# Optimization experiments

Hardware: AMD Instinct MI355X
Metric: run time of the kernel (lower is better)

Reference implementation:

```python
import jax, jax.numpy as jnp
import numpy as np

N = 100000     # nodes
H = 128        # hidden_channels == in_channels
OUT = 64       # out_channels
L = 3          # num_layers=4 -> num_layers-1 Layer modules
E = 1_600_000  # unique undirected edges (avg degree 16)
BN_EPS = 1e-5


def _make_edges():
    # Unique undirected edges, no self-loops -> dense symmetric adjacency in the
    # original module is exactly this edge set symmetrized.
    rng = np.random.default_rng(0)
    i = rng.integers(0, N, 1_700_000)
    j = rng.integers(0, N, 1_700_000)
    m = i != j
    i, j = i[m], j[m]
    lo, hi = np.minimum(i, j), np.maximum(i, j)
    pairs = np.unique(lo.astype(np.int64) * N + hi)[:E]
    lo = (pairs // N).astype(np.int32)
    hi = (pairs % N).astype(np.int32)
    src = jnp.asarray(np.concatenate([lo, hi]))  # [2E] directed
    dst = jnp.asarray(np.concatenate([hi, lo]))
    return src, dst


def setup_inputs() -> dict:
    key = jax.random.key(0)
    ks = jax.random.split(key, 24)
    nrm = lambda k, s: (jax.random.normal(k, s, dtype=jnp.float32) * 0.05)
    src, dst = _make_edges()
    return {
        "x": jax.random.normal(ks[0], (N, H), dtype=jnp.float32),
        "src": src,
        "dst": dst,
        # per-Layer MLP(in=H, hidden=H, out=H): Linear->ReLU->Linear, stacked over L
        "layer_W1": nrm(ks[1], (L, H, H)),
        "layer_b1": nrm(ks[2], (L, H)),
        "layer_W2": nrm(ks[3], (L, H, H)),
        "layer_b2": nrm(ks[4], (L, H)),
        # BatchNorm1d (eval mode: running stats)
        "bn_gamma": 1.0 + nrm(ks[5], (L, H)),
        "bn_beta": nrm(ks[6], (L, H)),
        "bn_mean": nrm(ks[7], (L, H)),
        "bn_var": jax.random.uniform(ks[8], (L, H), jnp.float32, 0.5, 1.5),
        # single shared GRUCell(H, H)
        "gru_Wih": nrm(ks[9], (3 * H, H)),
        "gru_Whh": nrm(ks[10], (3 * H, H)),
        "gru_bih": nrm(ks[11], (3 * H,)),
        "gru_bhh": nrm(ks[12], (3 * H,)),
        # mlp_last: MLP(H, H, OUT)
        "last_W1": nrm(ks[13], (H, H)),
        "last_b1": nrm(ks[14], (H,)),
        "last_W2": nrm(ks[15], (OUT, H)),
        "last_b2": nrm(ks[16], (OUT,)),
    }


def reference(x, src, dst, layer_W1, layer_b1, layer_W2, layer_b2,
              bn_gamma, bn_beta, bn_mean, bn_var,
              gru_Wih, gru_Whh, gru_bih, gru_bhh,
              last_W1, last_b1, last_W2, last_b2):
    n = x.shape[0]
    deg = jax.ops.segment_sum(jnp.ones(src.shape[0], x.dtype), dst, num_segments=n)
    inv_deg = (1.0 / jnp.maximum(deg, 1.0))[:, None]  # isolated nodes -> 0 agg
    h = jnp.zeros((n, H), x.dtype)
    for l in range(L):
        agg = jax.ops.segment_sum(x[src], dst, num_segments=n) * inv_deg  # mean over neighbors
        c = x + agg
        c = jnp.maximum(c @ layer_W1[l].T + layer_b1[l], 0.0) @ layer_W2[l].T + layer_b2[l]
        c = bn_gamma[l] * (c - bn_mean[l]) * jax.lax.rsqrt(bn_var[l] + BN_EPS) + bn_beta[l]
        # F.dropout(training=False) is identity
        gi = c @ gru_Wih.T + gru_bih  # [n, 3H]
        gh = h @ gru_Whh.T + gru_bhh
        r = jax.nn.sigmoid(gi[:, :H] + gh[:, :H])
        z = jax.nn.sigmoid(gi[:, H:2 * H] + gh[:, H:2 * H])
        nst = jnp.tanh(gi[:, 2 * H:] + r * gh[:, 2 * H:])
        h = (1.0 - z) * nst + z * h
        x = h
    return jnp.maximum(x @ last_W1.T + last_b1, 0.0) @ last_W2.T + last_b2
```

## Files before the change

### kernel.cpp

```cpp
#include <hip/hip_runtime.h>
#include <hip/hip_bf16.h>
#include <stdint.h>

typedef __bf16 bf16;
typedef __bf16 bf16x8 __attribute__((ext_vector_type(8)));
typedef float f32x4 __attribute__((ext_vector_type(4)));
typedef uint32_t u32x4 __attribute__((ext_vector_type(4)));

#define HD 128
#define LDP (HD + 8)
#define NTPB 4
#define MFMA __builtin_amdgcn_mfma_f32_16x16x32_bf16

__device__ inline float bflo(uint32_t u){ return __uint_as_float(u << 16); }
__device__ inline float bfhi(uint32_t u){ return __uint_as_float(u & 0xffff0000u); }
__device__ inline uint32_t packbf(float a, float b){
    bf16 x = (bf16)a, y = (bf16)b;
    uint16_t ux = __builtin_bit_cast(uint16_t, x), uy = __builtin_bit_cast(uint16_t, y);
    return (uint32_t)ux | ((uint32_t)uy << 16);
}
__device__ inline bf16x8 ldb8(const bf16* p){ return *(const bf16x8*)p; }
__device__ inline float sigm(float x){ return 1.f / (1.f + __expf(-x)); }
__device__ inline float tanh_fast(float x){ float t = __expf(-2.f * x); return (1.f - t) / (1.f + t); }
__device__ inline uint32_t swz(uint32_t b){ return b ^ (((b >> 8) & 7u) << 4); }

__global__ void k_cvt(const float* __restrict__ in, bf16* __restrict__ out, int n){
    int i = blockIdx.x * 256 + threadIdx.x;
    if (i < n) out[i] = (bf16)in[i];
}

__global__ void k_cvt_x(const float* __restrict__ in, uint32_t* __restrict__ out, int nU){
    int i = blockIdx.x * 256 + threadIdx.x;
    if (i >= nU) return;
    int r = i >> 6, dw = i & 63;
    uint32_t v = packbf(in[(size_t)i * 2], in[(size_t)i * 2 + 1]);
    int slot = dw >> 2, w = dw & 3;
    out[(size_t)r * 64 + (((slot ^ (r & 7)) << 2) | w)] = v;
}

__global__ void k_bound(const int* __restrict__ dstB, int E, int* __restrict__ rows2, int n){
    int v = blockIdx.x * 256 + threadIdx.x;
    if (v > n) return;
    int lo = 0, hi = E;
    while (lo < hi){ int mid = (lo + hi) >> 1; if (dstB[mid] < v) lo = mid + 1; else hi = mid; }
    rows2[v] = lo;
}

__global__ void k_count(const int* __restrict__ dst, int* __restrict__ deg, int ne){
    int i = blockIdx.x * 256 + threadIdx.x;
    if (i < ne) atomicAdd(&deg[dst[i]], 1);
}

__global__ void k_scan1(const int* __restrict__ deg, int* __restrict__ rows,
                        int* __restrict__ bsum, int n){
    __shared__ int lds[256];
    int b = blockIdx.x, tid = threadIdx.x;
    int i0 = b * 1024 + tid * 4;
    int v[4]; int s = 0;
#pragma unroll
    for (int j = 0; j < 4; ++j){ int idx = i0 + j; v[j] = (idx < n) ? deg[idx] : 0; s += v[j]; }
    lds[tid] = s; __syncthreads();
    int acc = s;
    for (int off = 1; off < 256; off <<= 1){
        int add = (tid >= off) ? lds[tid - off] : 0;
        __syncthreads();
        acc += add; lds[tid] = acc;
        __syncthreads();
    }
    int run = acc - s;
#pragma unroll
    for (int j = 0; j < 4; ++j){ int idx = i0 + j; if (idx < n) rows[idx] = run; run += v[j]; }
    if (tid == 255) bsum[b] = acc;
}

__global__ void k_scan2(int* __restrict__ bsum, int nb){
    __shared__ int lds[128];
    int tid = threadIdx.x;
    int v = (tid < nb) ? bsum[tid] : 0;
    lds[tid] = v; __syncthreads();
    int acc = v;
    for (int off = 1; off < 128; off <<= 1){
        int add = (tid >= off) ? lds[tid - off] : 0;
        __syncthreads();
        acc += add; lds[tid] = acc;
        __syncthreads();
    }
    if (tid < nb) bsum[tid] = acc - v;
}

__global__ void k_scan3(int* __restrict__ rows, const int* __restrict__ bsum, int n, int total){
    int i = blockIdx.x * 256 + threadIdx.x;
    if (i < n) rows[i] += bsum[i >> 10];
    if (i == n) rows[n] = total;
}

__global__ void k_fillp(const int* __restrict__ src, const int* __restrict__ dst,
                        int* __restrict__ cur, int* __restrict__ col, int ne, int nPerG){
    int g = blockIdx.x & 7;
    int i = (blockIdx.x >> 3) * 256 + threadIdx.x;
    if (i >= ne) return;
    int d = dst[i];
    int lo = g * nPerG;
    if (d >= lo && d < lo + nPerG){
        int p = atomicAdd(&cur[d], 1);
        col[p] = src[i];
    }
}

__global__ __launch_bounds__(256) void k_gather(
    const bf16* __restrict__ curx,
    const int* __restrict__ srcB, const int* __restrict__ rows2,
    const int* __restrict__ colB, const int* __restrict__ rowsB,
    bf16* __restrict__ cout, int n)
{
    int wid = threadIdx.x >> 6, lane = threadIdx.x & 63;
    int v = blockIdx.x * 4 + wid;
    if (v >= n) return;
    int grp = lane >> 3, sl = lane & 7;
    int a0 = rows2[v], a1 = rows2[v + 1];
    int b0 = rowsB[v], b1 = rowsB[v + 1];
    int deg = (a1 - a0) + (b1 - b0);
    float inv = (deg > 0) ? 1.f / (float)deg : 0.f;

    const u32x4* base = (const u32x4*)curx;
    float acc[16];
#pragma unroll
    for (int k = 0; k < 16; ++k) acc[k] = 0.f;

    for (int j = a0 + grp; j < a1; j += 8){
        int nb = srcB[j];
        int px = nb & 7;
        u32x4 q0 = base[(size_t)nb * 16 + (sl ^ px)];
        u32x4 q1 = base[(size_t)nb * 16 + 8 + (sl ^ px)];
#pragma unroll
        for (int k = 0; k < 4; ++k){
            acc[2*k]   += bflo(q0[k]); acc[2*k+1]   += bfhi(q0[k]);
            acc[8+2*k] += bflo(q1[k]); acc[8+2*k+1] += bfhi(q1[k]);
        }
    }
    for (int j = b0 + grp; j < b1; j += 8){
        int nb = colB[j];
        int px = nb & 7;
        u32x4 q0 = base[(size_t)nb * 16 + (sl ^ px)];
        u32x4 q1 = base[(size_t)nb * 16 + 8 + (sl ^ px)];
#pragma unroll
        for (int k = 0; k < 4; ++k){
            acc[2*k]   += bflo(q0[k]); acc[2*k+1]   += bfhi(q0[k]);
            acc[8+2*k] += bflo(q1[k]); acc[8+2*k+1] += bfhi(q1[k]);
        }
    }
#pragma unroll
    for (int k = 0; k < 16; ++k){
        acc[k] += __shfl_xor(acc[k], 8);
        acc[k] += __shfl_xor(acc[k], 16);
        acc[k] += __shfl_xor(acc[k], 32);
    }
    if (grp == 0){
        int pv = v & 7;
        u32x4 x0 = base[(size_t)v * 16 + (sl ^ pv)];
        u32x4 x1 = base[(size_t)v * 16 + 8 + (sl ^ pv)];
        u32x4 o0, o1;
#pragma unroll
        for (int k = 0; k < 4; ++k){
            o0[k] = packbf(bflo(x0[k]) + acc[2*k] * inv,   bfhi(x0[k]) + acc[2*k+1] * inv);
            o1[k] = packbf(bflo(x1[k]) + acc[8+2*k] * inv, bfhi(x1[k]) + acc[8+2*k+1] * inv);
        }
        ((u32x4*)cout)[(size_t)v * 16 + (sl ^ pv)]     = o0;
        ((u32x4*)cout)[(size_t)v * 16 + 8 + (sl ^ pv)] = o1;
    }
}

#define CL0 0u
#define CL1 32768u
#define HL0 65536u
#define ALO 98304u
__global__ __launch_bounds__(512, 1) void k_layer(
    const bf16* __restrict__ cin, const bf16* __restrict__ hOld, bf16* __restrict__ hNew,
    const bf16* __restrict__ W1, const float* __restrict__ b1,
    const bf16* __restrict__ W2, const float* __restrict__ b2,
    const float* __restrict__ gm, const float* __restrict__ bt,
    const float* __restrict__ mu, const float* __restrict__ vr,
    const bf16* __restrict__ Wih, const bf16* __restrict__ Whh,
    const float* __restrict__ bih, const float* __restrict__ bhh, int nT)
{
    __shared__ __align__(16) char smem[131072];
    int tid = threadIdx.x, wid = tid >> 6, lane = tid & 63;
    int rA = lane & 15, u = lane >> 4, ko = u * 8;
    int c = wid * 16 + rA;

    bf16x8 W1f[4], W2f[4], Gri[4], Grh[4], Gzi[4], Gzh[4], Gni[4], Gnh[4];
#pragma unroll
    for (int kk = 0; kk < 4; ++kk){
        W1f[kk] = ldb8(W1  + (size_t)c * HD + ko + kk * 32);
        W2f[kk] = ldb8(W2  + (size_t)c * HD + ko + kk * 32);
        Gri[kk] = ldb8(Wih + (size_t)c * HD + ko + kk * 32);
        Gzi[kk] = ldb8(Wih + (size_t)(c + 128) * HD + ko + kk * 32);
        Gni[kk] = ldb8(Wih + (size_t)(c + 256) * HD + ko + kk * 32);
        Grh[kk] = ldb8(Whh + (size_t)c * HD + ko + kk * 32);
        Gzh[kk] = ldb8(Whh + (size_t)(c + 128) * HD + ko + kk * 32);
        Gnh[kk] = ldb8(Whh + (size_t)(c + 256) * HD + ko + kk * 32);
    }
    float b1c = b1[c];
    float bnS = gm[c] * rsqrtf(vr[c] + 1e-5f);
    float bnO = bt[c] - mu[c] * bnS;
    float b2c = b2[c];
    float br = bih[c] + bhh[c], bz = bih[c + 128] + bhh[c + 128];
    float bin = bih[c + 256], bhn = bhh[c + 256];

    auto gload = [&](const char* g, uint32_t lo){
        __builtin_amdgcn_global_load_lds(
            (const __attribute__((address_space(1))) void*)g,
            (__attribute__((address_space(3))) void*)(smem + lo), 16, 0, 0);
    };
    auto stageC = [&](int t, uint32_t dst){
        const char* g = (const char*)cin + (size_t)t * 32768 + (size_t)lane * 16;
#pragma unroll
        for (int i = 0; i < 4; ++i){
            uint32_t ch = (uint32_t)(wid * 4 + i) * 1024;
            gload(g + ch, dst + ch);
        }
    };
    auto stageH = [&](int t){
        const char* g = (const char*)hOld + (size_t)t * 32768 + (size_t)lane * 16;
#pragma unroll
        for (int i = 0; i < 4; ++i){
            uint32_t ch = (uint32_t)(wid * 4 + i) * 1024;
            gload(g + ch, HL0 + ch);
        }
    };

    int t = blockIdx.x;
    int cur = 0;
    if (t < nT) stageC(t, CL0);
    for (; t < nT; t += (int)gridDim.x){
        __syncthreads();
        stageH(t);
        int tn = t + (int)gridDim.x;
        if (tn < nT) stageC(tn, cur ? CL0 : CL1);
        uint32_t CB = cur ? CL1 : CL0;

#pragma unroll
        for (int m = 0; m < 8; ++m){
            bf16x8 a_[4];
#pragma unroll
            for (int kk = 0; kk < 4; ++kk){
                uint32_t b = (uint32_t)(m * 16 + rA) * 256 + (uint32_t)(u * 16 + kk * 64);
                a_[kk] = *(const bf16x8*)(smem + CB + swz(b));
            }
            f32x4 acc = {0,0,0,0};
#pragma unroll
            for (int kk = 0; kk < 4; ++kk) acc = MFMA(a_[kk], W1f[kk], acc, 0, 0, 0);
#pragma unroll
            for (int j = 0; j < 4; ++j){
                uint32_t r = (uint32_t)(m * 16 + u * 4 + j);
                *(bf16*)(smem + ALO + swz(r * 256 + (uint32_t)c * 2)) =
                    (bf16)fmaxf(acc[j] + b1c, 0.f);
            }
        }
        asm volatile("s_waitcnt lgkmcnt(0)" ::: "memory");
        __builtin_amdgcn_sched_barrier(0);
        __builtin_amdgcn_s_barrier();

#pragma unroll
        for (int m = 0; m < 8; ++m){
            bf16x8 a_[4];
#pragma unroll
            for (int kk = 0; kk < 4; ++kk){
                uint32_t b = (uint32_t)(m * 16 + rA) * 256 + (uint32_t)(u * 16 + kk * 64);
                a_[kk] = *(const bf16x8*)(smem + ALO + swz(b));
            }
            f32x4 acc = {0,0,0,0};
#pragma unroll
            for (int kk = 0; kk < 4; ++kk) acc = MFMA(a_[kk], W2f[kk], acc, 0, 0, 0);
#pragma unroll
            for (int j = 0; j < 4; ++j){
                uint32_t r = (uint32_t)(m * 16 + u * 4 + j);
                *(bf16*)(smem + CB + swz(r * 256 + (uint32_t)c * 2)) =
                    (bf16)((acc[j] + b2c) * bnS + bnO);
            }
        }
        if (tn < nT){ asm volatile("s_waitcnt vmcnt(4) lgkmcnt(0)" ::: "memory"); }
        else        { asm volatile("s_waitcnt vmcnt(0) lgkmcnt(0)" ::: "memory"); }
        __builtin_amdgcn_sched_barrier(0);
        __builtin_amdgcn_s_barrier();

#pragma unroll
        for (int m = 0; m < 8; ++m){
            bf16x8 ac_[4], ah_[4];
#pragma unroll
            for (int kk = 0; kk < 4; ++kk){
                uint32_t b = (uint32_t)(m * 16 + rA) * 256 + (uint32_t)(u * 16 + kk * 64);
                ac_[kk] = *(const bf16x8*)(smem + CB + swz(b));
                ah_[kk] = *(const bf16x8*)(smem + HL0 + swz(b));
            }
            f32x4 rr = {0,0,0,0}, zz = {0,0,0,0}, gi = {0,0,0,0}, gh = {0,0,0,0};
#pragma unroll
            for (int kk = 0; kk < 4; ++kk){
                rr = MFMA(ac_[kk], Gri[kk], rr, 0, 0, 0);
                rr = MFMA(ah_[kk], Grh[kk], rr, 0, 0, 0);
                zz = MFMA(ac_[kk], Gzi[kk], zz, 0, 0, 0);
                zz = MFMA(ah_[kk], Gzh[kk], zz, 0, 0, 0);
                gi = MFMA(ac_[kk], Gni[kk], gi, 0, 0, 0);
                gh = MFMA(ah_[kk], Gnh[kk], gh, 0, 0, 0);
            }
#pragma unroll
            for (int j = 0; j < 4; ++j){
                uint32_t r = (uint32_t)(m * 16 + u * 4 + j);
                uint32_t inner = swz(r * 256 + (uint32_t)c * 2);
                float hold = (float)*(const bf16*)(smem + HL0 + inner);
                float rg = sigm(rr[j] + br);
                float zg = sigm(zz[j] + bz);
                float ng = tanh_fast(gi[j] + bin + rg * (gh[j] + bhn));
                *(bf16*)(smem + ALO + inner) = (bf16)((1.f - zg) * ng + zg * hold);
            }
        }
        asm volatile("s_waitcnt lgkmcnt(0)" ::: "memory");
        __builtin_amdgcn_sched_barrier(0);
        __builtin_amdgcn_s_barrier();

        {
            char* hNb = (char*)hNew + (size_t)t * 32768;
#pragma unroll
            for (int i = 0; i < 4; ++i){
                uint32_t off = (uint32_t)tid * 16 + (uint32_t)i * 8192;
                *(u32x4*)(hNb + off) = *(const u32x4*)(smem + ALO + off);
            }
        }
        cur ^= 1;
    }
}

__global__ __launch_bounds__(256) void k_final(
    const bf16* __restrict__ hin, const bf16* __restrict__ W1, const float* __restrict__ b1,
    const bf16* __restrict__ W2, const float* __restrict__ b2,
    float* __restrict__ out, int nTiles)
{
    __shared__ bf16 lds[NTPB][16][LDP];
    int wid = threadIdx.x >> 6, lane = threadIdx.x & 63;
    int tile = blockIdx.x * NTPB + wid;
    if (tile >= nTiles) return;
    int r0 = tile * 16;
    int rA = lane & 15, u = lane >> 4, ko = u * 8;

    bf16x8 a[4];
    const char* hb = (const char*)hin;
    uint32_t b0 = (uint32_t)(r0 + rA) * 256 + (uint32_t)(u * 16);
#pragma unroll
    for (int kk = 0; kk < 4; ++kk) a[kk] = *(const bf16x8*)(hb + swz(b0 + (uint32_t)kk * 64));

#pragma unroll
    for (int t = 0; t < 8; ++t){
        f32x4 acc = {0.f, 0.f, 0.f, 0.f};
        int c = t * 16 + rA;
        const bf16* bp = W1 + (size_t)c * HD + ko;
#pragma unroll
        for (int kk = 0; kk < 4; ++kk)
            acc = MFMA(a[kk], ldb8(bp + kk * 32), acc, 0, 0, 0);
        float bias = b1[c];
#pragma unroll
        for (int j = 0; j < 4; ++j){
            float v = fmaxf(acc[j] + bias, 0.f);
            lds[wid][u * 4 + j][c] = (bf16)v;
        }
    }
    __threadfence_block();
    bf16x8 a2[4];
    const bf16* lp = &lds[wid][rA][ko];
#pragma unroll
    for (int kk = 0; kk < 4; ++kk) a2[kk] = ldb8(lp + kk * 32);

#pragma unroll
    for (int t = 0; t < 4; ++t){
        f32x4 acc = {0.f, 0.f, 0.f, 0.f};
        int c = t * 16 + rA;
        const bf16* bp = W2 + (size_t)c * HD + ko;
#pragma unroll
        for (int kk = 0; kk < 4; ++kk)
            acc = MFMA(a2[kk], ldb8(bp + kk * 32), acc, 0, 0, 0);
        float bias = b2[c];
#pragma unroll
        for (int j = 0; j < 4; ++j)
            out[(size_t)(r0 + u * 4 + j) * 64 + c] = acc[j] + bias;
    }
}

extern "C" void kernel_launch(void* const* d_in, const int* in_sizes, int n_in,
                              void* d_out, int out_size, void* d_ws, size_t ws_size,
                              hipStream_t stream)
{
    const float* x    = (const float*)d_in[0];
    const int*   src  = (const int*)d_in[1];
    const int*   dst  = (const int*)d_in[2];
    const float* lW1  = (const float*)d_in[3];
    const float* lb1  = (const float*)d_in[4];
    const float* lW2  = (const float*)d_in[5];
    const float* lb2  = (const float*)d_in[6];
    const float* gmm  = (const float*)d_in[7];
    const float* bta  = (const float*)d_in[8];
    const float* mun  = (const float*)d_in[9];
    const float* vrr  = (const float*)d_in[10];
    const float* Wih  = (const float*)d_in[11];
    const float* Whh  = (const float*)d_in[12];
    const float* bih  = (const float*)d_in[13];
    const float* bhh  = (const float*)d_in[14];
    const float* fW1  = (const float*)d_in[15];
    const float* fb1  = (const float*)d_in[16];
    const float* fW2  = (const float*)d_in[17];
    const float* fb2  = (const float*)d_in[18];

    int n  = in_sizes[0] / HD;
    int ne = in_sizes[1];
    int E  = ne / 2;
    int L  = in_sizes[3] / (HD * HD);
    int nPad = (n + 127) & ~127;

    char* w = (char*)d_ws;
    auto alloc = [&](size_t bytes) -> char* {
        char* p = w; w += (bytes + 255) & ~(size_t)255; return p;
    };
    bf16* xbf  = (bf16*)alloc((size_t)nPad * HD * 2);
    bf16* hA   = (bf16*)alloc((size_t)nPad * HD * 2);
    bf16* hB   = (bf16*)alloc((size_t)nPad * HD * 2);
    bf16* cin  = (bf16*)alloc((size_t)nPad * HD * 2);
    bf16* W1b  = (bf16*)alloc((size_t)L * HD * HD * 2);
    bf16* W2b  = (bf16*)alloc((size_t)L * HD * HD * 2);
    bf16* Wib  = (bf16*)alloc((size_t)3 * HD * HD * 2);
    bf16* Whb  = (bf16*)alloc((size_t)3 * HD * HD * 2);
    bf16* fW1b = (bf16*)alloc((size_t)HD * HD * 2);
    bf16* fW2b = (bf16*)alloc((size_t)64 * HD * 2);
    int*  degB = (int*)alloc((size_t)n * 4);
    int*  rowsB= (int*)alloc((size_t)(n + 1) * 4);
    int*  rows2= (int*)alloc((size_t)(n + 1) * 4);
    int*  bsum = (int*)alloc(512);
    int*  curB = (int*)alloc((size_t)n * 4);
    int*  colB = (int*)alloc((size_t)E * 4);

    auto cvt = [&](const float* i, bf16* o, int cnt){
        k_cvt<<<(cnt + 255) / 256, 256, 0, stream>>>(i, o, cnt);
    };
    int nU = n * 64;
    k_cvt_x<<<(nU + 255) / 256, 256, 0, stream>>>(x, (uint32_t*)xbf, nU);
    cvt(lW1, W1b,  L * HD * HD);
    cvt(lW2, W2b,  L * HD * HD);
    cvt(Wih, Wib,  3 * HD * HD);
    cvt(Whh, Whb,  3 * HD * HD);
    cvt(fW1, fW1b, HD * HD);
    cvt(fW2, fW2b, 64 * HD);

    hipMemsetAsync(degB, 0, (size_t)n * 4, stream);
    hipMemsetAsync(hA, 0, (size_t)nPad * HD * 2, stream);

    k_bound<<<(n + 1 + 255) / 256, 256, 0, stream>>>(dst + E, E, rows2, n);
    k_count<<<(E + 255) / 256, 256, 0, stream>>>(dst, degB, E);
    int nb = (n + 1023) / 1024;
    k_scan1<<<nb, 256, 0, stream>>>(degB, rowsB, bsum, n);
    k_scan2<<<1, 128, 0, stream>>>(bsum, nb);
    k_scan3<<<(n + 1 + 255) / 256, 256, 0, stream>>>(rowsB, bsum, n, E);
    hipMemcpyAsync(curB, rowsB, (size_t)n * 4, hipMemcpyDeviceToDevice, stream);
    int nPerG = (n + 7) / 8;
    k_fillp<<<8 * ((E + 255) / 256), 256, 0, stream>>>(src, dst, curB, colB, E, nPerG);

    int nT128 = nPad / 128;
    int nT16 = (n + 15) / 16;
    int gF = (nT16 + NTPB - 1) / NTPB;

    const bf16* curp = xbf;
    for (int l = 0; l < L; ++l){
        k_gather<<<(n + 3) / 4, 256, 0, stream>>>(curp, src + E, rows2, colB, rowsB, cin, n);
        k_layer<<<256, 512, 0, stream>>>(cin, hA, hB,
            W1b + (size_t)l * HD * HD, lb1 + l * HD,
            W2b + (size_t)l * HD * HD, lb2 + l * HD,
            gmm + l * HD, bta + l * HD, mun + l * HD, vrr + l * HD,
            Wib, Whb, bih, bhh, nT128);
        bf16* tmp = hA; hA = hB; hB = tmp;
        curp = hA;
    }
    k_final<<<gF, 256, 0, stream>>>(hA, fW1b, fb1, fW2b, fb2, (float*)d_out, nT16);
}
```

Before: 764.3 us.

## Shrink layer tiles to 64 rows and run multiple blocks per CU

Halves the per-tile row count in the fused MLP+BN+GRU layer kernel, cutting shared memory from 128 KB to 48 KB. Launch bounds now request 4 blocks per CU and the grid grows to 768 blocks. The old double-buffered C staging is replaced by single buffers: the next tile's C and H are loaded after the GRU phase and waited on at the loop end. The aim is to hide latency by running more blocks at once rather than by in-block prefetch. The tighter launch bound caps VGPRs per thread, while the kernel keeps 32 bf16x8 weight fragments resident, so register spills are a risk.

```diff
diff --git a/kernel.cpp b/kernel.cpp
--- a/kernel.cpp
+++ b/kernel.cpp
@@ -170,11 +170,11 @@
     }
 }
 
-#define CL0 0u
-#define CL1 32768u
-#define HL0 65536u
-#define ALO 98304u
-__global__ __launch_bounds__(512, 1) void k_layer(
+#define NR   64
+#define CBUF 0u
+#define HBUF 16384u
+#define ABUF 32768u
+__global__ __launch_bounds__(512, 4) void k_layer(
     const bf16* __restrict__ cin, const bf16* __restrict__ hOld, bf16* __restrict__ hNew,
     const bf16* __restrict__ W1, const float* __restrict__ b1,
     const bf16* __restrict__ W2, const float* __restrict__ b2,
@@ -183,7 +183,7 @@
     const bf16* __restrict__ Wih, const bf16* __restrict__ Whh,
     const float* __restrict__ bih, const float* __restrict__ bhh, int nT)
 {
-    __shared__ __align__(16) char smem[131072];
+    __shared__ __align__(16) char smem[49152];
     int tid = threadIdx.x, wid = tid >> 6, lane = tid & 63;
     int rA = lane & 15, u = lane >> 4, ko = u * 8;
     int c = wid * 16 + rA;
@@ -212,40 +212,37 @@
             (const __attribute__((address_space(1))) void*)g,
             (__attribute__((address_space(3))) void*)(smem + lo), 16, 0, 0);
     };
-    auto stageC = [&](int t, uint32_t dst){
-        const char* g = (const char*)cin + (size_t)t * 32768 + (size_t)lane * 16;
-#pragma unroll
-        for (int i = 0; i < 4; ++i){
-            uint32_t ch = (uint32_t)(wid * 4 + i) * 1024;
-            gload(g + ch, dst + ch);
+    auto stageC = [&](int t){
+        const char* g = (const char*)cin + (size_t)t * 16384 + (size_t)lane * 16;
+#pragma unroll
+        for (int i = 0; i < 2; ++i){
+            uint32_t ch = (uint32_t)(wid * 2 + i) * 1024;
+            gload(g + ch, CBUF + ch);
         }
     };
     auto stageH = [&](int t){
-        const char* g = (const char*)hOld + (size_t)t * 32768 + (size_t)lane * 16;
-#pragma unroll
-        for (int i = 0; i < 4; ++i){
-            uint32_t ch = (uint32_t)(wid * 4 + i) * 1024;
-            gload(g + ch, HL0 + ch);
+        const char* g = (const char*)hOld + (size_t)t * 16384 + (size_t)lane * 16;
+#pragma unroll
+        for (int i = 0; i < 2; ++i){
+            uint32_t ch = (uint32_t)(wid * 2 + i) * 1024;
+            gload(g + ch, HBUF + ch);
         }
     };
 
-    int t = blockIdx.x;
-    int cur = 0;
-    if (t < nT) stageC(t, CL0);
-    for (; t < nT; t += (int)gridDim.x){
-        __syncthreads();
-        stageH(t);
-        int tn = t + (int)gridDim.x;
-        if (tn < nT) stageC(tn, cur ? CL0 : CL1);
-        uint32_t CB = cur ? CL1 : CL0;
-
-#pragma unroll
-        for (int m = 0; m < 8; ++m){
+    int t0 = blockIdx.x;
+    if (t0 < nT){ stageC(t0); stageH(t0); }
+    asm volatile("s_waitcnt vmcnt(0) lgkmcnt(0)" ::: "memory");
+    __builtin_amdgcn_sched_barrier(0);
+    __builtin_amdgcn_s_barrier();
+
+    for (int t = t0; t < nT; t += (int)gridDim.x){
+#pragma unroll
+        for (int m = 0; m < 4; ++m){
             bf16x8 a_[4];
 #pragma unroll
             for (int kk = 0; kk < 4; ++kk){
                 uint32_t b = (uint32_t)(m * 16 + rA) * 256 + (uint32_t)(u * 16 + kk * 64);
-                a_[kk] = *(const bf16x8*)(smem + CB + swz(b));
+                a_[kk] = *(const bf16x8*)(smem + CBUF + swz(b));
             }
             f32x4 acc = {0,0,0,0};
 #pragma unroll
@@ -253,7 +250,7 @@
 #pragma unroll
             for (int j = 0; j < 4; ++j){
                 uint32_t r = (uint32_t)(m * 16 + u * 4 + j);
-                *(bf16*)(smem + ALO + swz(r * 256 + (uint32_t)c * 2)) =
+                *(bf16*)(smem + ABUF + swz(r * 256 + (uint32_t)c * 2)) =
                     (bf16)fmaxf(acc[j] + b1c, 0.f);
             }
         }
@@ -262,12 +259,12 @@
         __builtin_amdgcn_s_barrier();
 
 #pragma unroll
-        for (int m = 0; m < 8; ++m){
+        for (int m = 0; m < 4; ++m){
             bf16x8 a_[4];
 #pragma unroll
             for (int kk = 0; kk < 4; ++kk){
                 uint32_t b = (uint32_t)(m * 16 + rA) * 256 + (uint32_t)(u * 16 + kk * 64);
-                a_[kk] = *(const bf16x8*)(smem + ALO + swz(b));
+                a_[kk] = *(const bf16x8*)(smem + ABUF + swz(b));
             }
             f32x4 acc = {0,0,0,0};
 #pragma unroll
@@ -275,23 +272,22 @@
 #pragma unroll
             for (int j = 0; j < 4; ++j){
                 uint32_t r = (uint32_t)(m * 16 + u * 4 + j);
-                *(bf16*)(smem + CB + swz(r * 256 + (uint32_t)c * 2)) =
+                *(bf16*)(smem + CBUF + swz(r * 256 + (uint32_t)c * 2)) =
                     (bf16)((acc[j] + b2c) * bnS + bnO);
             }
         }
-        if (tn < nT){ asm volatile("s_waitcnt vmcnt(4) lgkmcnt(0)" ::: "memory"); }
-        else        { asm volatile("s_waitcnt vmcnt(0) lgkmcnt(0)" ::: "memory"); }
+        asm volatile("s_waitcnt lgkmcnt(0)" ::: "memory");
         __builtin_amdgcn_sched_barrier(0);
         __builtin_amdgcn_s_barrier();
 
 #pragma unroll
-        for (int m = 0; m < 8; ++m){
+        for (int m = 0; m < 4; ++m){
             bf16x8 ac_[4], ah_[4];
 #pragma unroll
             for (int kk = 0; kk < 4; ++kk){
                 uint32_t b = (uint32_t)(m * 16 + rA) * 256 + (uint32_t)(u * 16 + kk * 64);
-                ac_[kk] = *(const bf16x8*)(smem + CB + swz(b));
-                ah_[kk] = *(const bf16x8*)(smem + HL0 + swz(b));
+                ac_[kk] = *(const bf16x8*)(smem + CBUF + swz(b));
+                ah_[kk] = *(const bf16x8*)(smem + HBUF + swz(b));
             }
             f32x4 rr = {0,0,0,0}, zz = {0,0,0,0}, gi = {0,0,0,0}, gh = {0,0,0,0};
 #pragma unroll
@@ -307,26 +303,30 @@
             for (int j = 0; j < 4; ++j){
                 uint32_t r = (uint32_t)(m * 16 + u * 4 + j);
                 uint32_t inner = swz(r * 256 + (uint32_t)c * 2);
-                float hold = (float)*(const bf16*)(smem + HL0 + inner);
+                float hold = (float)*(const bf16*)(smem + HBUF + inner);
                 float rg = sigm(rr[j] + br);
                 float zg = sigm(zz[j] + bz);
                 float ng = tanh_fast(gi[j] + bin + rg * (gh[j] + bhn));
-                *(bf16*)(smem + ALO + inner) = (bf16)((1.f - zg) * ng + zg * hold);
+                *(bf16*)(smem + ABUF + inner) = (bf16)((1.f - zg) * ng + zg * hold);
             }
         }
         asm volatile("s_waitcnt lgkmcnt(0)" ::: "memory");
         __builtin_amdgcn_sched_barrier(0);
         __builtin_amdgcn_s_barrier();
 
+        int tn = t + (int)gridDim.x;
+        if (tn < nT){ stageC(tn); stageH(tn); }
         {
-            char* hNb = (char*)hNew + (size_t)t * 32768;
-#pragma unroll
-            for (int i = 0; i < 4; ++i){
+            char* hNb = (char*)hNew + (size_t)t * 16384;
+#pragma unroll
+            for (int i = 0; i < 2; ++i){
                 uint32_t off = (uint32_t)tid * 16 + (uint32_t)i * 8192;
-                *(u32x4*)(hNb + off) = *(const u32x4*)(smem + ALO + off);
-            }
-        }
-        cur ^= 1;
+                *(u32x4*)(hNb + off) = *(const u32x4*)(smem + ABUF + off);
+            }
+        }
+        asm volatile("s_waitcnt vmcnt(2) lgkmcnt(0)" ::: "memory");
+        __builtin_amdgcn_sched_barrier(0);
+        __builtin_amdgcn_s_barrier();
     }
 }
 
@@ -460,18 +460,20 @@
     int nPerG = (n + 7) / 8;
     k_fillp<<<8 * ((E + 255) / 256), 256, 0, stream>>>(src, dst, curB, colB, E, nPerG);
 
-    int nT128 = nPad / 128;
+    int nT64 = nPad / 64;
+    int gL = 768;
+    if (gL > nT64) gL = nT64;
     int nT16 = (n + 15) / 16;
     int gF = (nT16 + NTPB - 1) / NTPB;
 
     const bf16* curp = xbf;
     for (int l = 0; l < L; ++l){
         k_gather<<<(n + 3) / 4, 256, 0, stream>>>(curp, src + E, rows2, colB, rowsB, cin, n);
-        k_layer<<<256, 512, 0, stream>>>(cin, hA, hB,
+        k_layer<<<gL, 512, 0, stream>>>(cin, hA, hB,
             W1b + (size_t)l * HD * HD, lb1 + l * HD,
             W2b + (size_t)l * HD * HD, lb2 + l * HD,
             gmm + l * HD, bta + l * HD, mun + l * HD, vrr + l * HD,
-            Wib, Whb, bih, bhh, nT128);
+            Wib, Whb, bih, bhh, nT64);
         bf16* tmp = hA; hA = hB; hB = tmp;
         curp = hA;
     }
```

Result: slower. 1.175 ms (+53.7%).
